# Performance work log

Hardware: AMD Instinct MI355X
Metric: run time of the kernel (lower is better)

Reference implementation:

```python
import jax, jax.numpy as jnp
import numpy as np

BN_EPS = 1e-5
NEG_SLOPE = 0.2


def _add_self_loops(edge_index, n):
    loops = jnp.arange(n, dtype=edge_index.dtype)
    src = jnp.concatenate([edge_index[0], loops])
    dst = jnp.concatenate([edge_index[1], loops])
    return src, dst


def _batchnorm(h, g, b):
    mean = h.mean(axis=0)
    var = h.var(axis=0)  # biased, as in BN forward
    return (h - mean) * jax.lax.rsqrt(var + BN_EPS) * g + b


def _gat_conv(x, edge_index, W, att_src, att_dst, bias):
    # heads=2, concat=False (mean over heads), add_self_loops=True
    n = x.shape[0]
    H, F = att_src.shape
    xp = (x @ W).reshape(n, H, F)                      # [N,H,F]
    a_src = jnp.einsum('nhf,hf->nh', xp, att_src)      # [N,H]
    a_dst = jnp.einsum('nhf,hf->nh', xp, att_dst)
    src, dst = _add_self_loops(edge_index, n)
    e = jax.nn.leaky_relu(a_src[src] + a_dst[dst], NEG_SLOPE)  # [Et,H]
    emax = jax.ops.segment_max(e, dst, num_segments=n)[dst]
    ex = jnp.exp(e - emax)
    denom = jax.ops.segment_sum(ex, dst, num_segments=n)[dst]
    alpha = ex / denom                                 # softmax per dst node
    msg = xp[src] * alpha[..., None]                   # [Et,H,F]
    out = jax.ops.segment_sum(msg, dst, num_segments=n)
    return out.mean(axis=1) + bias                     # [N,F]


def _gcn_conv(x, edge_index, W, bias):
    n = x.shape[0]
    xp = x @ W
    src, dst = _add_self_loops(edge_index, n)
    deg = jax.ops.segment_sum(jnp.ones_like(src, dtype=xp.dtype), dst, num_segments=n)
    dinv = jnp.where(deg > 0, jax.lax.rsqrt(jnp.maximum(deg, 1.0)), 0.0)
    norm = dinv[src] * dinv[dst]                       # [Et]
    out = jax.ops.segment_sum(xp[src] * norm[:, None], dst, num_segments=n)
    return out + bias


def setup_inputs() -> dict:
    key = jax.random.key(0)
    ks = jax.random.split(key, 16)
    N, E, D_IN, HID, LAT, DEC = 50000, 800000, 256, 128, 64, 256
    s = lambda fan: 1.0 / np.sqrt(fan)
    inp = {
        'x': jax.random.normal(ks[0], (N, D_IN), jnp.float32),
        'edge_index': jax.random.randint(ks[1], (2, E), 0, N, dtype=jnp.int32),
        'gat_W': jax.random.normal(ks[2], (D_IN, 2 * HID), jnp.float32) * s(D_IN),
        'gat_att_src': jax.random.normal(ks[3], (2, HID), jnp.float32) * s(HID),
        'gat_att_dst': jax.random.normal(ks[4], (2, HID), jnp.float32) * s(HID),
        'gat_bias': jnp.zeros((HID,), jnp.float32),
        'bn1_g': jnp.ones((HID,), jnp.float32),
        'bn1_b': jnp.zeros((HID,), jnp.float32),
        'gcn_W': jax.random.normal(ks[5], (HID, LAT), jnp.float32) * s(HID),
        'gcn_bias': jnp.zeros((LAT,), jnp.float32),
        'bn2_g': jnp.ones((LAT,), jnp.float32),
        'bn2_b': jnp.zeros((LAT,), jnp.float32),
        'mu_W': jax.random.normal(ks[6], (LAT, LAT), jnp.float32) * s(LAT),
        'mu_b': jnp.zeros((LAT,), jnp.float32),
        'lv_W': jax.random.normal(ks[7], (LAT, LAT), jnp.float32) * s(LAT),
        'lv_b': jnp.zeros((LAT,), jnp.float32),
        'res_W': jax.random.normal(ks[8], (LAT, LAT), jnp.float32) * s(LAT),
        'res_b': jnp.zeros((LAT,), jnp.float32),
        'dec_W1': jax.random.normal(ks[9], (2 * LAT, DEC), jnp.float32) * s(2 * LAT),
        'dec_b1': jnp.zeros((DEC,), jnp.float32),
        'dec_W2': jax.random.normal(ks[10], (DEC, 1), jnp.float32) * s(DEC),
        'dec_b2': jnp.zeros((1,), jnp.float32),
        'eps': jax.random.normal(ks[11], (N, LAT), jnp.float32),
    }
    return inp


def reference(x, edge_index, gat_W, gat_att_src, gat_att_dst, gat_bias,
              bn1_g, bn1_b, gcn_W, gcn_bias, bn2_g, bn2_b,
              mu_W, mu_b, lv_W, lv_b, res_W, res_b,
              dec_W1, dec_b1, dec_W2, dec_b2, eps):
    # encode (dropout omitted: eval mode; BN uses batch statistics)
    h = jax.nn.relu(_gat_conv(x, edge_index, gat_W, gat_att_src, gat_att_dst, gat_bias))
    h = _batchnorm(h, bn1_g, bn1_b)
    h = jax.nn.relu(_gcn_conv(h, edge_index, gcn_W, gcn_bias))
    h = _batchnorm(h, bn2_g, bn2_b)
    mu = h @ mu_W + mu_b
    logvar = h @ lv_W + lv_b
    # reparameterize
    z = mu + eps * jnp.exp(0.5 * logvar)
    # decode: edge-gather -> residual linear -> concat -> MLP
    res_z = z @ res_W + res_b
    row, col = edge_index[0], edge_index[1]
    e_emb = jnp.concatenate([res_z[row], res_z[col]], axis=1)  # [E, 2*LAT]
    hdec = jax.nn.relu(e_emb @ dec_W1 + dec_b1)
    recon = (hdec @ dec_W2 + dec_b2)[:, 0]
    return recon, mu, logvar
```

## Files before the change

kernel.cpp:

```cpp
#include <hip/hip_runtime.h>
#include <math.h>

constexpr int DIN = 256;
constexpr int HID = 128;
constexpr int LAT = 64;

typedef short bfrag __attribute__((ext_vector_type(8)));
typedef float f32x4 __attribute__((ext_vector_type(4)));

__device__ __forceinline__ float4 ld4(const float* p) { return *reinterpret_cast<const float4*>(p); }
__device__ __forceinline__ void st4(float* p, float4 v) { *reinterpret_cast<float4*>(p) = v; }

__device__ __forceinline__ unsigned short f2bf(float f) {
  unsigned int u = __float_as_uint(f);
  unsigned int r = (u + 0x7FFFu + ((u >> 16) & 1u)) >> 16;
  return (unsigned short)r;
}

__device__ __forceinline__ float bf2f(unsigned short u) {
  return __uint_as_float(((unsigned int)u) << 16);
}

__global__ __launch_bounds__(256) void gemm64(const float* __restrict__ A, const float* __restrict__ B,
                                              const float* __restrict__ crow, float* __restrict__ C,
                                              int M, int N, int K) {
  __shared__ float As[32][68];
  __shared__ float Bs[32][68];
  int t = threadIdx.x;
  int m0 = blockIdx.x * 64, n0 = blockIdx.y * 64;
  int tm = t & 15, tn = t >> 4;
  float acc[4][4];
#pragma unroll
  for (int i = 0; i < 4; i++)
#pragma unroll
    for (int j = 0; j < 4; j++) acc[i][j] = 0.f;

  for (int kt = 0; kt < K; kt += 32) {
#pragma unroll
    for (int i = 0; i < 2; ++i) {
      int f4 = t + i * 256;
      int m = f4 >> 3;
      int k4 = (f4 & 7) << 2;
      int gm = m0 + m;
      float4 v = make_float4(0.f, 0.f, 0.f, 0.f);
      if (gm < M) v = ld4(A + (size_t)gm * K + kt + k4);
      As[k4 + 0][m] = v.x; As[k4 + 1][m] = v.y; As[k4 + 2][m] = v.z; As[k4 + 3][m] = v.w;
    }
#pragma unroll
    for (int i = 0; i < 2; ++i) {
      int f4 = t + i * 256;
      int k = f4 >> 4;
      int n4 = (f4 & 15) << 2;
      float4 v = ld4(B + (size_t)(kt + k) * N + n0 + n4);
      st4(&Bs[k][n4], v);
    }
    __syncthreads();
#pragma unroll
    for (int k = 0; k < 32; ++k) {
      float4 a = ld4(&As[k][tm << 2]);
      float4 b = ld4(&Bs[k][tn << 2]);
      float av[4] = {a.x, a.y, a.z, a.w};
      float bv[4] = {b.x, b.y, b.z, b.w};
#pragma unroll
      for (int i = 0; i < 4; i++)
#pragma unroll
        for (int j = 0; j < 4; j++) acc[i][j] = fmaf(av[i], bv[j], acc[i][j]);
    }
    __syncthreads();
  }
#pragma unroll
  for (int i = 0; i < 4; ++i) {
    int gm = m0 + (tm << 2) + i;
    if (gm < M) {
      int nb = n0 + (tn << 2);
      float4 v = make_float4(acc[i][0], acc[i][1], acc[i][2], acc[i][3]);
      if (crow) { v.x += crow[nb]; v.y += crow[nb + 1]; v.z += crow[nb + 2]; v.w += crow[nb + 3]; }
      st4(C + (size_t)gm * N + nb, v);
    }
  }
}

__global__ __launch_bounds__(256) void gemm64b(const float* __restrict__ A, const float* __restrict__ B,
                                               const float* __restrict__ crow, unsigned short* __restrict__ Cb,
                                               int M, int N, int K) {
  __shared__ float As[32][68];
  __shared__ float Bs[32][68];
  int t = threadIdx.x;
  int m0 = blockIdx.x * 64, n0 = blockIdx.y * 64;
  int tm = t & 15, tn = t >> 4;
  float acc[4][4];
#pragma unroll
  for (int i = 0; i < 4; i++)
#pragma unroll
    for (int j = 0; j < 4; j++) acc[i][j] = 0.f;

  for (int kt = 0; kt < K; kt += 32) {
#pragma unroll
    for (int i = 0; i < 2; ++i) {
      int f4 = t + i * 256;
      int m = f4 >> 3;
      int k4 = (f4 & 7) << 2;
      int gm = m0 + m;
      float4 v = make_float4(0.f, 0.f, 0.f, 0.f);
      if (gm < M) v = ld4(A + (size_t)gm * K + kt + k4);
      As[k4 + 0][m] = v.x; As[k4 + 1][m] = v.y; As[k4 + 2][m] = v.z; As[k4 + 3][m] = v.w;
    }
#pragma unroll
    for (int i = 0; i < 2; ++i) {
      int f4 = t + i * 256;
      int k = f4 >> 4;
      int n4 = (f4 & 15) << 2;
      float4 v = ld4(B + (size_t)(kt + k) * N + n0 + n4);
      st4(&Bs[k][n4], v);
    }
    __syncthreads();
#pragma unroll
    for (int k = 0; k < 32; ++k) {
      float4 a = ld4(&As[k][tm << 2]);
      float4 b = ld4(&Bs[k][tn << 2]);
      float av[4] = {a.x, a.y, a.z, a.w};
      float bv[4] = {b.x, b.y, b.z, b.w};
#pragma unroll
      for (int i = 0; i < 4; i++)
#pragma unroll
        for (int j = 0; j < 4; j++) acc[i][j] = fmaf(av[i], bv[j], acc[i][j]);
    }
    __syncthreads();
  }
#pragma unroll
  for (int i = 0; i < 4; ++i) {
    int gm = m0 + (tm << 2) + i;
    if (gm < M) {
      int nb = n0 + (tn << 2);
      ushort4 o;
      o.x = f2bf(acc[i][0] + crow[nb]);
      o.y = f2bf(acc[i][1] + crow[nb + 1]);
      o.z = f2bf(acc[i][2] + crow[nb + 2]);
      o.w = f2bf(acc[i][3] + crow[nb + 3]);
      *(ushort4*)(Cb + (size_t)gm * N + nb) = o;
    }
  }
}

__global__ __launch_bounds__(256) void gemm_xp_mfma(const float* __restrict__ xf,
                                                    const unsigned short* __restrict__ Wtb,
                                                    unsigned short* __restrict__ xpb, int M) {
  __shared__ unsigned short Als[64 * 256];
  __shared__ unsigned short Bls[64 * 256];
  int t = threadIdx.x;
  int wv = t >> 6, l = t & 63, lg = l >> 4, ll = l & 15;
  int cg = blockIdx.x;
  int rt = blockIdx.y;

  {
    int row = t >> 2, seg = t & 3;
    int gr = min(rt * 64 + row, M - 1);
    const float4* src = (const float4*)(xf + (size_t)gr * 256 + seg * 64);
    int swz = (row & 7) << 4;
#pragma unroll
    for (int c = 0; c < 8; ++c) {
      float4 a = src[2 * c], b = src[2 * c + 1];
      uint4 v;
      v.x = (unsigned)f2bf(a.x) | ((unsigned)f2bf(a.y) << 16);
      v.y = (unsigned)f2bf(a.z) | ((unsigned)f2bf(a.w) << 16);
      v.z = (unsigned)f2bf(b.x) | ((unsigned)f2bf(b.y) << 16);
      v.w = (unsigned)f2bf(b.z) | ((unsigned)f2bf(b.w) << 16);
      int bo = seg * 128 + c * 16;
      *(uint4*)((char*)Als + row * 512 + (bo ^ swz)) = v;
    }
  }
  {
    int col = t >> 2, seg = t & 3;
    const uint4* src = (const uint4*)(Wtb + (size_t)(cg * 64 + col) * 256 + seg * 64);
    int swz = (col & 7) << 4;
#pragma unroll
    for (int c = 0; c < 8; ++c) {
      int bo = seg * 128 + c * 16;
      *(uint4*)((char*)Bls + col * 512 + (bo ^ swz)) = src[c];
    }
  }
  __syncthreads();

  f32x4 acc[4];
#pragma unroll
  for (int i = 0; i < 4; ++i) acc[i] = (f32x4){0.f, 0.f, 0.f, 0.f};

#pragma unroll
  for (int kt = 0; kt < 8; ++kt) {
    int ar = wv * 16 + ll;
    bfrag af = *(const bfrag*)((char*)Als + ar * 512 + ((kt * 64 + lg * 16) ^ ((ar & 7) << 4)));
#pragma unroll
    for (int fn = 0; fn < 4; ++fn) {
      int bc = fn * 16 + ll;
      bfrag bf = *(const bfrag*)((char*)Bls + bc * 512 + ((kt * 64 + lg * 16) ^ ((bc & 7) << 4)));
      acc[fn] = __builtin_amdgcn_mfma_f32_16x16x32_bf16(af, bf, acc[fn], 0, 0, 0);
    }
  }

#pragma unroll
  for (int fn = 0; fn < 4; ++fn) {
#pragma unroll
    for (int r = 0; r < 4; ++r) {
      int row = rt * 64 + wv * 16 + lg * 4 + r;
      if (row < M) xpb[(size_t)row * 512 + cg * 64 + fn * 16 + ll] = f2bf(acc[fn][r]);
    }
  }
}

__global__ __launch_bounds__(256) void attn_scores_bf(const unsigned short* __restrict__ xpb,
                                                      const float* __restrict__ att_src,
                                                      const float* __restrict__ att_dst,
                                                      float* __restrict__ a_src, float* __restrict__ a_dst, int N) {
  int wid = threadIdx.x >> 6, lane = threadIdx.x & 63;
  int n = blockIdx.x * 4 + wid;
  if (n >= N) return;
  int h = lane >> 5;
  int f4 = (lane & 31) << 2;
  ushort4 u = *(const ushort4*)(xpb + (size_t)n * 512 + lane * 4);
  float4 as = ld4(att_src + h * 128 + f4);
  float4 ad = ld4(att_dst + h * 128 + f4);
  float vx = bf2f(u.x), vy = bf2f(u.y), vz = bf2f(u.z), vw = bf2f(u.w);
  float ps = vx * as.x + vy * as.y + vz * as.z + vw * as.w;
  float pd = vx * ad.x + vy * ad.y + vz * ad.z + vw * ad.w;
#pragma unroll
  for (int m = 16; m >= 1; m >>= 1) { ps += __shfl_xor(ps, m); pd += __shfl_xor(pd, m); }
  if ((lane & 31) == 0) { a_src[n * 2 + h] = ps; a_dst[n * 2 + h] = pd; }
}

__global__ void deg_count(const int* __restrict__ ei, int E, int Et, int* __restrict__ deg) {
  int i = blockIdx.x * blockDim.x + threadIdx.x;
  if (i >= Et) return;
  int d = (i < E) ? ei[E + i] : (i - E);
  atomicAdd(&deg[d], 1);
}

__global__ __launch_bounds__(256) void bsum_kernel(const int* __restrict__ deg, int N, int* __restrict__ bsum) {
  int t = threadIdx.x;
  int i = blockIdx.x * 256 + t;
  int v = (i < N) ? deg[i] : 0;
#pragma unroll
  for (int m = 32; m >= 1; m >>= 1) v += __shfl_xor(v, m);
  __shared__ int sh[4];
  if ((t & 63) == 0) sh[t >> 6] = v;
  __syncthreads();
  if (t == 0) bsum[blockIdx.x] = sh[0] + sh[1] + sh[2] + sh[3];
}

__global__ __launch_bounds__(256) void bscan_kernel(int* __restrict__ bsum, int B) {
  __shared__ int sh[256];
  int t = threadIdx.x;
  int v = (t < B) ? bsum[t] : 0;
  sh[t] = v;
  __syncthreads();
  for (int d = 1; d < 256; d <<= 1) {
    int x = (t >= d) ? sh[t - d] : 0;
    __syncthreads();
    sh[t] += x;
    __syncthreads();
  }
  if (t < B) bsum[t] = sh[t] - v;
}

__global__ __launch_bounds__(256) void scan_apply(const int* __restrict__ deg, const int* __restrict__ bsum, int N,
                                                  int* __restrict__ offs, int* __restrict__ cursor,
                                                  float* __restrict__ dinv) {
  int t = threadIdx.x;
  int i = blockIdx.x * 256 + t;
  int v = (i < N) ? deg[i] : 0;
  __shared__ int sh[256];
  sh[t] = v;
  __syncthreads();
  for (int d = 1; d < 256; d <<= 1) {
    int x = (t >= d) ? sh[t - d] : 0;
    __syncthreads();
    sh[t] += x;
    __syncthreads();
  }
  if (i < N) {
    int off = bsum[blockIdx.x] + sh[t] - v;
    offs[i] = off;
    cursor[i] = off;
    dinv[i] = rsqrtf((float)v);
  }
}

__global__ void csr_fill(const int* __restrict__ ei, int E, int Et, int* __restrict__ cursor, int* __restrict__ csr) {
  int i = blockIdx.x * blockDim.x + threadIdx.x;
  if (i >= Et) return;
  int s, d;
  if (i < E) { s = ei[i]; d = ei[E + i]; } else { s = i - E; d = i - E; }
  int pos = atomicAdd(&cursor[d], 1);
  csr[pos] = s;
}

__global__ __launch_bounds__(256) void gat_fused(const int* __restrict__ offs, const int* __restrict__ deg,
                                                 const int* __restrict__ csr, const float* __restrict__ a_src,
                                                 const float* __restrict__ a_dst,
                                                 const unsigned short* __restrict__ xpb,
                                                 const float* __restrict__ bias,
                                                 float* __restrict__ h1, int N) {
  int wid = threadIdx.x >> 6, lane = threadIdx.x & 63;
  int n = blockIdx.x * 4 + wid;
  if (n >= N) return;
  int off = offs[n], dg = deg[n];
  float ad0 = a_dst[n * 2], ad1 = a_dst[n * 2 + 1];
  const float2* as2 = (const float2*)a_src;

  float4 acc = make_float4(0.f, 0.f, 0.f, 0.f);
  float s0 = 0.f, s1 = 0.f;
  bool h0 = lane < 32;

#define GAT_STEP(aa, uu)                                         \
  {                                                              \
    float e0 = (aa).x + ad0; e0 = e0 >= 0.f ? e0 : 0.2f * e0;    \
    float e1 = (aa).y + ad1; e1 = e1 >= 0.f ? e1 : 0.2f * e1;    \
    float x0 = __expf(e0), x1 = __expf(e1);                      \
    s0 += x0; s1 += x1;                                          \
    float xa = h0 ? x0 : x1;                                     \
    acc.x = fmaf(bf2f((uu).x), xa, acc.x);                       \
    acc.y = fmaf(bf2f((uu).y), xa, acc.y);                       \
    acc.z = fmaf(bf2f((uu).z), xa, acc.z);                       \
    acc.w = fmaf(bf2f((uu).w), xa, acc.w);                       \
  }

  int k = 0;
  for (; k + 4 <= dg; k += 4) {
    int sa = csr[off + k], sb = csr[off + k + 1], sc = csr[off + k + 2], sd = csr[off + k + 3];
    float2 aa = as2[sa], ab = as2[sb], ac = as2[sc], ad = as2[sd];
    ushort4 ua = ((const ushort4*)(xpb + (size_t)sa * 512))[lane];
    ushort4 ub = ((const ushort4*)(xpb + (size_t)sb * 512))[lane];
    ushort4 uc = ((const ushort4*)(xpb + (size_t)sc * 512))[lane];
    ushort4 ud = ((const ushort4*)(xpb + (size_t)sd * 512))[lane];
    GAT_STEP(aa, ua); GAT_STEP(ab, ub); GAT_STEP(ac, uc); GAT_STEP(ad, ud);
  }
  for (; k < dg; ++k) {
    int s = csr[off + k];
    float2 a = as2[s];
    ushort4 u = ((const ushort4*)(xpb + (size_t)s * 512))[lane];
    GAT_STEP(a, u);
  }
#undef GAT_STEP

  float r = h0 ? (1.f / s0) : (1.f / s1);
  acc.x *= r; acc.y *= r; acc.z *= r; acc.w *= r;

  float ox = __shfl_down(acc.x, 32);
  float oy = __shfl_down(acc.y, 32);
  float oz = __shfl_down(acc.z, 32);
  float ow = __shfl_down(acc.w, 32);
  if (h0) {
    int f4 = lane << 2;
    float4 b = ld4(bias + f4);
    float4 o;
    o.x = fmaxf(0.f, (acc.x + ox) * 0.5f + b.x);
    o.y = fmaxf(0.f, (acc.y + oy) * 0.5f + b.y);
    o.z = fmaxf(0.f, (acc.z + oz) * 0.5f + b.z);
    o.w = fmaxf(0.f, (acc.w + ow) * 0.5f + b.w);
    st4(h1 + (size_t)n * 128 + f4, o);
  }
}

template <int C>
__global__ __launch_bounds__(256) void bn_stats(const float* __restrict__ h, int N, float* __restrict__ P,
                                                float* __restrict__ PS) {
  constexpr int R = 256 / C;
  __shared__ float sh[256], sh2[256];
  int t = threadIdx.x;
  int c = t % C, r = t / C;
  float s = 0.f, ss = 0.f;
  for (int n = blockIdx.x * R + r; n < N; n += gridDim.x * R) {
    float v = h[(size_t)n * C + c];
    s += v; ss += v * v;
  }
  sh[t] = s; sh2[t] = ss;
  __syncthreads();
  if (r == 0) {
#pragma unroll
    for (int i = 1; i < R; ++i) { s += sh[i * C + c]; ss += sh2[i * C + c]; }
    P[blockIdx.x * C + c] = s;
    PS[blockIdx.x * C + c] = ss;
  }
}

__global__ __launch_bounds__(256) void bn_fold_gcn(const float* __restrict__ P, const float* __restrict__ PS,
                                                   int G, int N, const float* __restrict__ g,
                                                   const float* __restrict__ b, const float* __restrict__ W,
                                                   float* __restrict__ Wf, float* __restrict__ cvec) {
  __shared__ float ssv[128], stv[128];
  int t = threadIdx.x;
  if (t < 128) {
    float s = 0.f, ss = 0.f;
    for (int i = 0; i < G; ++i) { s += P[i * 128 + t]; ss += PS[i * 128 + t]; }
    float mean = s / N;
    float var = ss / N - mean * mean;
    float sc = g[t] * rsqrtf(var + 1e-5f);
    ssv[t] = sc;
    stv[t] = b[t] - mean * sc;
  }
  __syncthreads();
  for (int i = t; i < 128 * 64; i += 256) {
    int k = i >> 6;
    Wf[i] = ssv[k] * W[i];
  }
  if (t < 64) {
    float c = 0.f;
    for (int k = 0; k < 128; ++k) c += stv[k] * W[k * 64 + t];
    cvec[t] = c;
  }
}

__global__ __launch_bounds__(256) void bn_fold_mulv(const float* __restrict__ P, const float* __restrict__ PS,
                                                    int G, int N, const float* __restrict__ g,
                                                    const float* __restrict__ b,
                                                    const float* __restrict__ Wmu, const float* __restrict__ mub,
                                                    const float* __restrict__ Wlv, const float* __restrict__ lvb,
                                                    float* __restrict__ Wmuf, float* __restrict__ cmu,
                                                    float* __restrict__ Wlvf, float* __restrict__ clv) {
  __shared__ float ssv[64], stv[64];
  int t = threadIdx.x;
  if (t < 64) {
    float s = 0.f, ss = 0.f;
    for (int i = 0; i < G; ++i) { s += P[i * 64 + t]; ss += PS[i * 64 + t]; }
    float mean = s / N;
    float var = ss / N - mean * mean;
    float sc = g[t] * rsqrtf(var + 1e-5f);
    ssv[t] = sc;
    stv[t] = b[t] - mean * sc;
  }
  __syncthreads();
  for (int i = t; i < 4096; i += 256) {
    int k = i >> 6;
    Wmuf[i] = ssv[k] * Wmu[i];
    Wlvf[i] = ssv[k] * Wlv[i];
  }
  if (t < 64) {
    float cm = mub[t], cl = lvb[t];
    for (int k = 0; k < 64; ++k) { cm += stv[k] * Wmu[k * 64 + t]; cl += stv[k] * Wlv[k * 64 + t]; }
    cmu[t] = cm; clv[t] = cl;
  }
}

__global__ __launch_bounds__(256) void gcn_aggregate_bf(const int* __restrict__ offs, const int* __restrict__ deg,
                                                        const int* __restrict__ csr,
                                                        const unsigned short* __restrict__ xpb2,
                                                        const float* __restrict__ dinv, const float* __restrict__ bias,
                                                        float* __restrict__ g2, int N) {
  int wid = threadIdx.x >> 6, lane = threadIdx.x & 63;
  int n = blockIdx.x * 4 + wid;
  if (n >= N) return;
  int off = offs[n], dg = deg[n];
  float acc = 0.f;
  int k = 0;
  for (; k + 4 <= dg; k += 4) {
    int sa = csr[off + k], sb = csr[off + k + 1], sc = csr[off + k + 2], sd = csr[off + k + 3];
    float da = dinv[sa], db = dinv[sb], dc = dinv[sc], dd = dinv[sd];
    unsigned short ua = xpb2[(size_t)sa * 64 + lane];
    unsigned short ub = xpb2[(size_t)sb * 64 + lane];
    unsigned short uc = xpb2[(size_t)sc * 64 + lane];
    unsigned short ud = xpb2[(size_t)sd * 64 + lane];
    acc = fmaf(bf2f(ua), da, acc);
    acc = fmaf(bf2f(ub), db, acc);
    acc = fmaf(bf2f(uc), dc, acc);
    acc = fmaf(bf2f(ud), dd, acc);
  }
  for (; k < dg; ++k) {
    int s = csr[off + k];
    acc = fmaf(bf2f(xpb2[(size_t)s * 64 + lane]), dinv[s], acc);
  }
  float v = acc * dinv[n] + bias[lane];
  g2[(size_t)n * 64 + lane] = fmaxf(v, 0.f);
}

__global__ void reparam(const float* __restrict__ mu, const float* __restrict__ lv,
                        const float* __restrict__ eps, float* __restrict__ z, int total) {
  int i = blockIdx.x * blockDim.x + threadIdx.x;
  if (i >= total) return;
  z[i] = fmaf(eps[i], __expf(0.5f * lv[i]), mu[i]);
}

__global__ void prep_gatW(const float* __restrict__ W, unsigned short* __restrict__ Wtb) {
  int i = blockIdx.x * blockDim.x + threadIdx.x;
  if (i >= 256 * 256) return;
  int col = i >> 8, k = i & 255;
  Wtb[i] = f2bf(W[k * 256 + col]);
}

__global__ void prep_W1(const float* __restrict__ W1, unsigned short* __restrict__ W1t) {
  int i = blockIdx.x * blockDim.x + threadIdx.x;
  if (i >= 4 * 256 * 40) return;
  int kt = i / 10240;
  int rem = i - kt * 10240;
  int j = rem / 40;
  int kp = rem - j * 40;
  float v = (kp < 32) ? W1[(size_t)(kt * 32 + kp) * 256 + j] : 0.f;
  W1t[i] = f2bf(v);
}

__global__ __launch_bounds__(256) void decoder_mfma(const int* __restrict__ ei, int E,
                                                    const unsigned short* __restrict__ rzb,
                                                    const unsigned short* __restrict__ W1t,
                                                    const float* __restrict__ b1, const float* __restrict__ W2,
                                                    const float* __restrict__ b2, float* __restrict__ recon) {
  __shared__ unsigned short Als[64 * 128];
  __shared__ unsigned short Bls[256 * 40];
  __shared__ float red[4][64];
  int t = threadIdx.x;
  int wv = t >> 6, l = t & 63;
  int lg = l >> 4, ll = l & 15;
  int e0 = blockIdx.x * 64;

  {
    int e = t >> 2;
    int part = (t >> 1) & 1;
    int half = t & 1;
    int eg = e0 + e;
    if (eg >= E) eg = E - 1;
    int r = (part == 0) ? ei[eg] : ei[E + eg];
    const uint4* gsrc = (const uint4*)(rzb + (size_t)r * 64 + half * 32);
    int bo0 = part * 128 + half * 64;
    int swz = (e & 7) << 4;
#pragma unroll
    for (int c = 0; c < 4; ++c) {
      uint4 v = gsrc[c];
      int bo = bo0 + c * 16;
      *(uint4*)&Als[e * 128 + ((bo ^ swz) >> 1)] = v;
    }
  }

  f32x4 acc[4][4];
#pragma unroll
  for (int a = 0; a < 4; ++a)
#pragma unroll
    for (int b = 0; b < 4; ++b) acc[a][b] = (f32x4){0.f, 0.f, 0.f, 0.f};

  for (int kt = 0; kt < 4; ++kt) {
    __syncthreads();
    {
      const uint4* gsrc = (const uint4*)(W1t + kt * 10240);
      uint4* ldst = (uint4*)Bls;
#pragma unroll
      for (int i = 0; i < 5; ++i) ldst[t + i * 256] = gsrc[t + i * 256];
    }
    __syncthreads();

    bfrag af[4];
#pragma unroll
    for (int fm = 0; fm < 4; ++fm) {
      int e = fm * 16 + ll;
      int bo = kt * 64 + lg * 16;
      af[fm] = *(const bfrag*)&Als[e * 128 + ((bo ^ ((e & 7) << 4)) >> 1)];
    }
#pragma unroll
    for (int fn = 0; fn < 4; ++fn) {
      int j = wv * 64 + fn * 16 + ll;
      bfrag bf = *(const bfrag*)&Bls[j * 40 + lg * 8];
#pragma unroll
      for (int fm = 0; fm < 4; ++fm)
        acc[fm][fn] = __builtin_amdgcn_mfma_f32_16x16x32_bf16(af[fm], bf, acc[fm][fn], 0, 0, 0);
    }
  }

  float bj[4], wj[4];
#pragma unroll
  for (int fn = 0; fn < 4; ++fn) {
    int j = wv * 64 + fn * 16 + ll;
    bj[fn] = b1[j];
    wj[fn] = W2[j];
  }
#pragma unroll
  for (int fm = 0; fm < 4; ++fm) {
    float pr[4] = {0.f, 0.f, 0.f, 0.f};
#pragma unroll
    for (int fn = 0; fn < 4; ++fn) {
#pragma unroll
      for (int r = 0; r < 4; ++r)
        pr[r] = fmaf(fmaxf(acc[fm][fn][r] + bj[fn], 0.f), wj[fn], pr[r]);
    }
#pragma unroll
    for (int m = 8; m >= 1; m >>= 1) {
#pragma unroll
      for (int r = 0; r < 4; ++r) pr[r] += __shfl_xor(pr[r], m);
    }
    if (ll == 0) {
#pragma unroll
      for (int r = 0; r < 4; ++r) red[wv][fm * 16 + lg * 4 + r] = pr[r];
    }
  }
  __syncthreads();
  if (t < 64) {
    int eg = e0 + t;
    if (eg < E) recon[eg] = red[0][t] + red[1][t] + red[2][t] + red[3][t] + b2[0];
  }
}

extern "C" void kernel_launch(void* const* d_in, const int* in_sizes, int n_in,
                              void* d_out, int out_size, void* d_ws, size_t ws_size,
                              hipStream_t stream) {
  const float* x = (const float*)d_in[0];
  const int* ei = (const int*)d_in[1];
  const float* gat_W = (const float*)d_in[2];
  const float* att_src = (const float*)d_in[3];
  const float* att_dst = (const float*)d_in[4];
  const float* gat_bias = (const float*)d_in[5];
  const float* bn1_g = (const float*)d_in[6];
  const float* bn1_b = (const float*)d_in[7];
  const float* gcn_W = (const float*)d_in[8];
  const float* gcn_bias = (const float*)d_in[9];
  const float* bn2_g = (const float*)d_in[10];
  const float* bn2_b = (const float*)d_in[11];
  const float* mu_W = (const float*)d_in[12];
  const float* mu_b = (const float*)d_in[13];
  const float* lv_W = (const float*)d_in[14];
  const float* lv_b = (const float*)d_in[15];
  const float* res_W = (const float*)d_in[16];
  const float* res_b = (const float*)d_in[17];
  const float* dec_W1 = (const float*)d_in[18];
  const float* dec_b1 = (const float*)d_in[19];
  const float* dec_W2 = (const float*)d_in[20];
  const float* dec_b2 = (const float*)d_in[21];
  const float* eps = (const float*)d_in[22];

  int N = in_sizes[0] / DIN;
  int E = in_sizes[1] / 2;
  int Et = E + N;
  int NB = (N + 255) / 256;

  float* ws = (float*)d_ws;
  size_t off = 0;
  float* xp = ws; off += (size_t)N * 256;
  unsigned short* xpb = (unsigned short*)xp;
  unsigned short* xpb2 = (unsigned short*)xp;
  float* g2 = xp + (size_t)N * 64;
  float* zb = xp + (size_t)N * 128;
  float* rz = xp + (size_t)N * 192;
  unsigned short* rzb = (unsigned short*)rz;
  float* h1 = ws + off; off += (size_t)N * 128;
  float* a_src = ws + off; off += (size_t)2 * N;
  float* a_dst = ws + off; off += (size_t)2 * N;
  float* dinv = ws + off; off += N;
  float* P = ws + off; off += 128 * 128;
  float* PS = ws + off; off += 128 * 128;
  float* W2f = ws + off; off += 128 * 64;
  float* c2 = ws + off; off += 64;
  float* Wmuf = ws + off; off += 64 * 64;
  float* cmu = ws + off; off += 64;
  float* Wlvf = ws + off; off += 64 * 64;
  float* clv = ws + off; off += 64;
  unsigned short* W1t = (unsigned short*)(ws + off); off += 20480;
  unsigned short* Wtb = (unsigned short*)(ws + off); off += 32768;
  int* deg = (int*)(ws + off); off += N;
  int* offs = (int*)(ws + off); off += N;
  int* cursor = (int*)(ws + off); off += N;
  int* bsum = (int*)(ws + off); off += 256;
  int* csr = (int*)(ws + off); off += Et;

  float* recon = (float*)d_out;
  float* mu = recon + E;
  float* lv = mu + (size_t)N * LAT;

  prep_W1<<<(4 * 256 * 40 + 255) / 256, 256, 0, stream>>>(dec_W1, W1t);
  prep_gatW<<<(256 * 256 + 255) / 256, 256, 0, stream>>>(gat_W, Wtb);

  dim3 gX(4, (N + 63) / 64);
  gemm_xp_mfma<<<gX, 256, 0, stream>>>(x, Wtb, xpb, N);

  attn_scores_bf<<<(N + 3) / 4, 256, 0, stream>>>(xpb, att_src, att_dst, a_src, a_dst, N);

  hipMemsetAsync(deg, 0, (size_t)N * sizeof(int), stream);
  deg_count<<<(Et + 255) / 256, 256, 0, stream>>>(ei, E, Et, deg);
  bsum_kernel<<<NB, 256, 0, stream>>>(deg, N, bsum);
  bscan_kernel<<<1, 256, 0, stream>>>(bsum, NB);
  scan_apply<<<NB, 256, 0, stream>>>(deg, bsum, N, offs, cursor, dinv);
  csr_fill<<<(Et + 255) / 256, 256, 0, stream>>>(ei, E, Et, cursor, csr);

  gat_fused<<<(N + 3) / 4, 256, 0, stream>>>(offs, deg, csr, a_src, a_dst, xpb, gat_bias, h1, N);

  bn_stats<128><<<128, 256, 0, stream>>>(h1, N, P, PS);
  bn_fold_gcn<<<1, 256, 0, stream>>>(P, PS, 128, N, bn1_g, bn1_b, gcn_W, W2f, c2);
  dim3 gB((N + 63) / 64, 1);
  gemm64b<<<gB, 256, 0, stream>>>(h1, W2f, c2, xpb2, N, 64, 128);

  gcn_aggregate_bf<<<(N + 3) / 4, 256, 0, stream>>>(offs, deg, csr, xpb2, dinv, gcn_bias, g2, N);

  bn_stats<64><<<128, 256, 0, stream>>>(g2, N, P, PS);
  bn_fold_mulv<<<1, 256, 0, stream>>>(P, PS, 128, N, bn2_g, bn2_b, mu_W, mu_b, lv_W, lv_b,
                                      Wmuf, cmu, Wlvf, clv);
  gemm64<<<gB, 256, 0, stream>>>(g2, Wmuf, cmu, mu, N, 64, 64);
  gemm64<<<gB, 256, 0, stream>>>(g2, Wlvf, clv, lv, N, 64, 64);

  reparam<<<(N * 64 + 255) / 256, 256, 0, stream>>>(mu, lv, eps, zb, N * 64);
  gemm64b<<<gB, 256, 0, stream>>>(zb, res_W, res_b, rzb, N, 64, 64);

  decoder_mfma<<<(E + 63) / 64, 256, 0, stream>>>(ei, E, rzb, W1t, dec_b1, dec_W2, dec_b2, recon);
}
```

Measured before the change: 574.5 us.

## Fuse attention scores into GAT GEMM, fuse mu/logvar/reparam/residual tail, unroll gathers

Computes the GAT attention source and destination scores in the GEMM epilogue from fp32 accumulators. Partial sums across column tiles are combined with atomicAdd into zero-initialised buffers, so the separate score kernel and its re-read of xp go away. Replaces the two mu/logvar GEMMs, the reparam kernel and the residual GEMM with one tail kernel that keeps z in shared memory. It also adds 8-way unrolled gather loops in the GAT and GCN aggregation kernels for more memory-level parallelism, at the cost of extra launch memset, atomics and register pressure.

```diff
diff --git a/kernel.cpp b/kernel.cpp
--- a/kernel.cpp
+++ b/kernel.cpp
@@ -19,65 +19,6 @@
 
 __device__ __forceinline__ float bf2f(unsigned short u) {
   return __uint_as_float(((unsigned int)u) << 16);
-}
-
-__global__ __launch_bounds__(256) void gemm64(const float* __restrict__ A, const float* __restrict__ B,
-                                              const float* __restrict__ crow, float* __restrict__ C,
-                                              int M, int N, int K) {
-  __shared__ float As[32][68];
-  __shared__ float Bs[32][68];
-  int t = threadIdx.x;
-  int m0 = blockIdx.x * 64, n0 = blockIdx.y * 64;
-  int tm = t & 15, tn = t >> 4;
-  float acc[4][4];
-#pragma unroll
-  for (int i = 0; i < 4; i++)
-#pragma unroll
-    for (int j = 0; j < 4; j++) acc[i][j] = 0.f;
-
-  for (int kt = 0; kt < K; kt += 32) {
-#pragma unroll
-    for (int i = 0; i < 2; ++i) {
-      int f4 = t + i * 256;
-      int m = f4 >> 3;
-      int k4 = (f4 & 7) << 2;
-      int gm = m0 + m;
-      float4 v = make_float4(0.f, 0.f, 0.f, 0.f);
-      if (gm < M) v = ld4(A + (size_t)gm * K + kt + k4);
-      As[k4 + 0][m] = v.x; As[k4 + 1][m] = v.y; As[k4 + 2][m] = v.z; As[k4 + 3][m] = v.w;
-    }
-#pragma unroll
-    for (int i = 0; i < 2; ++i) {
-      int f4 = t + i * 256;
-      int k = f4 >> 4;
-      int n4 = (f4 & 15) << 2;
-      float4 v = ld4(B + (size_t)(kt + k) * N + n0 + n4);
-      st4(&Bs[k][n4], v);
-    }
-    __syncthreads();
-#pragma unroll
-    for (int k = 0; k < 32; ++k) {
-      float4 a = ld4(&As[k][tm << 2]);
-      float4 b = ld4(&Bs[k][tn << 2]);
-      float av[4] = {a.x, a.y, a.z, a.w};
-      float bv[4] = {b.x, b.y, b.z, b.w};
-#pragma unroll
-      for (int i = 0; i < 4; i++)
-#pragma unroll
-        for (int j = 0; j < 4; j++) acc[i][j] = fmaf(av[i], bv[j], acc[i][j]);
-    }
-    __syncthreads();
-  }
-#pragma unroll
-  for (int i = 0; i < 4; ++i) {
-    int gm = m0 + (tm << 2) + i;
-    if (gm < M) {
-      int nb = n0 + (tn << 2);
-      float4 v = make_float4(acc[i][0], acc[i][1], acc[i][2], acc[i][3]);
-      if (crow) { v.x += crow[nb]; v.y += crow[nb + 1]; v.z += crow[nb + 2]; v.w += crow[nb + 3]; }
-      st4(C + (size_t)gm * N + nb, v);
-    }
-  }
 }
 
 __global__ __launch_bounds__(256) void gemm64b(const float* __restrict__ A, const float* __restrict__ B,
@@ -144,7 +85,10 @@
 
 __global__ __launch_bounds__(256) void gemm_xp_mfma(const float* __restrict__ xf,
                                                     const unsigned short* __restrict__ Wtb,
-                                                    unsigned short* __restrict__ xpb, int M) {
+                                                    const float* __restrict__ att_src,
+                                                    const float* __restrict__ att_dst,
+                                                    unsigned short* __restrict__ xpb,
+                                                    float* __restrict__ a_src, float* __restrict__ a_dst, int M) {
   __shared__ unsigned short Als[64 * 256];
   __shared__ unsigned short Bls[64 * 256];
   int t = threadIdx.x;
@@ -205,26 +149,38 @@
       if (row < M) xpb[(size_t)row * 512 + cg * 64 + fn * 16 + ll] = f2bf(acc[fn][r]);
     }
   }
-}
-
-__global__ __launch_bounds__(256) void attn_scores_bf(const unsigned short* __restrict__ xpb,
-                                                      const float* __restrict__ att_src,
-                                                      const float* __restrict__ att_dst,
-                                                      float* __restrict__ a_src, float* __restrict__ a_dst, int N) {
-  int wid = threadIdx.x >> 6, lane = threadIdx.x & 63;
-  int n = blockIdx.x * 4 + wid;
-  if (n >= N) return;
-  int h = lane >> 5;
-  int f4 = (lane & 31) << 2;
-  ushort4 u = *(const ushort4*)(xpb + (size_t)n * 512 + lane * 4);
-  float4 as = ld4(att_src + h * 128 + f4);
-  float4 ad = ld4(att_dst + h * 128 + f4);
-  float vx = bf2f(u.x), vy = bf2f(u.y), vz = bf2f(u.z), vw = bf2f(u.w);
-  float ps = vx * as.x + vy * as.y + vz * as.z + vw * as.w;
-  float pd = vx * ad.x + vy * ad.y + vz * ad.z + vw * ad.w;
-#pragma unroll
-  for (int m = 16; m >= 1; m >>= 1) { ps += __shfl_xor(ps, m); pd += __shfl_xor(pd, m); }
-  if ((lane & 31) == 0) { a_src[n * 2 + h] = ps; a_dst[n * 2 + h] = pd; }
+
+  int h = cg >> 1;
+  int c0 = (cg & 1) * 64;
+  float asv[4], adv[4];
+#pragma unroll
+  for (int fn = 0; fn < 4; ++fn) {
+    asv[fn] = att_src[h * 128 + c0 + fn * 16 + ll];
+    adv[fn] = att_dst[h * 128 + c0 + fn * 16 + ll];
+  }
+  float ps[4] = {0.f, 0.f, 0.f, 0.f}, pd[4] = {0.f, 0.f, 0.f, 0.f};
+#pragma unroll
+  for (int fn = 0; fn < 4; ++fn)
+#pragma unroll
+    for (int r = 0; r < 4; ++r) {
+      ps[r] = fmaf(acc[fn][r], asv[fn], ps[r]);
+      pd[r] = fmaf(acc[fn][r], adv[fn], pd[r]);
+    }
+#pragma unroll
+  for (int m = 8; m >= 1; m >>= 1) {
+#pragma unroll
+    for (int r = 0; r < 4; ++r) { ps[r] += __shfl_xor(ps[r], m); pd[r] += __shfl_xor(pd[r], m); }
+  }
+  if (ll == 0) {
+#pragma unroll
+    for (int r = 0; r < 4; ++r) {
+      int row = rt * 64 + wv * 16 + lg * 4 + r;
+      if (row < M) {
+        atomicAdd(&a_src[row * 2 + h], ps[r]);
+        atomicAdd(&a_dst[row * 2 + h], pd[r]);
+      }
+    }
+  }
 }
 
 __global__ void deg_count(const int* __restrict__ ei, int E, int Et, int* __restrict__ deg) {
@@ -324,6 +280,19 @@
   }
 
   int k = 0;
+  for (; k + 8 <= dg; k += 8) {
+    int s_[8];
+#pragma unroll
+    for (int q = 0; q < 8; ++q) s_[q] = csr[off + k + q];
+    float2 a_[8];
+    ushort4 u_[8];
+#pragma unroll
+    for (int q = 0; q < 8; ++q) a_[q] = as2[s_[q]];
+#pragma unroll
+    for (int q = 0; q < 8; ++q) u_[q] = ((const ushort4*)(xpb + (size_t)s_[q] * 512))[lane];
+#pragma unroll
+    for (int q = 0; q < 8; ++q) GAT_STEP(a_[q], u_[q]);
+  }
   for (; k + 4 <= dg; k += 4) {
     int sa = csr[off + k], sb = csr[off + k + 1], sc = csr[off + k + 2], sd = csr[off + k + 3];
     float2 aa = as2[sa], ab = as2[sb], ac = as2[sc], ad = as2[sd];
@@ -451,6 +420,19 @@
   int off = offs[n], dg = deg[n];
   float acc = 0.f;
   int k = 0;
+  for (; k + 8 <= dg; k += 8) {
+    int s_[8];
+#pragma unroll
+    for (int q = 0; q < 8; ++q) s_[q] = csr[off + k + q];
+    float d_[8];
+    unsigned short u_[8];
+#pragma unroll
+    for (int q = 0; q < 8; ++q) d_[q] = dinv[s_[q]];
+#pragma unroll
+    for (int q = 0; q < 8; ++q) u_[q] = xpb2[(size_t)s_[q] * 64 + lane];
+#pragma unroll
+    for (int q = 0; q < 8; ++q) acc = fmaf(bf2f(u_[q]), d_[q], acc);
+  }
   for (; k + 4 <= dg; k += 4) {
     int sa = csr[off + k], sb = csr[off + k + 1], sc = csr[off + k + 2], sd = csr[off + k + 3];
     float da = dinv[sa], db = dinv[sb], dc = dinv[sc], dd = dinv[sd];
@@ -471,11 +453,120 @@
   g2[(size_t)n * 64 + lane] = fmaxf(v, 0.f);
 }
 
-__global__ void reparam(const float* __restrict__ mu, const float* __restrict__ lv,
-                        const float* __restrict__ eps, float* __restrict__ z, int total) {
-  int i = blockIdx.x * blockDim.x + threadIdx.x;
-  if (i >= total) return;
-  z[i] = fmaf(eps[i], __expf(0.5f * lv[i]), mu[i]);
+__global__ __launch_bounds__(256) void tail_fused(const float* __restrict__ g2,
+                                                  const float* __restrict__ Wmuf, const float* __restrict__ cmu,
+                                                  const float* __restrict__ Wlvf, const float* __restrict__ clv,
+                                                  const float* __restrict__ resW, const float* __restrict__ resb,
+                                                  const float* __restrict__ eps,
+                                                  float* __restrict__ mu, float* __restrict__ lv,
+                                                  unsigned short* __restrict__ rzb, int N) {
+  __shared__ float Gs[64][68];
+  __shared__ float Wm[64][64];
+  __shared__ float Wl[64][64];
+  __shared__ float Rw[64][64];
+  int t = threadIdx.x;
+  int m0 = blockIdx.x * 64;
+  int tm = t & 15, tn = t >> 4;
+
+#pragma unroll
+  for (int i = 0; i < 4; ++i) {
+    int f4 = t + i * 256;
+    int row = f4 >> 4;
+    int k4 = (f4 & 15) << 2;
+    int gr = m0 + row;
+    float4 v = make_float4(0.f, 0.f, 0.f, 0.f);
+    if (gr < N) v = ld4(g2 + (size_t)gr * 64 + k4);
+    Gs[k4 + 0][row] = v.x; Gs[k4 + 1][row] = v.y; Gs[k4 + 2][row] = v.z; Gs[k4 + 3][row] = v.w;
+    st4(&Wm[f4 >> 4][k4], ld4(Wmuf + f4 * 4));
+    st4(&Wl[f4 >> 4][k4], ld4(Wlvf + f4 * 4));
+    st4(&Rw[f4 >> 4][k4], ld4(resW + f4 * 4));
+  }
+  __syncthreads();
+
+  float am[4][4], al[4][4];
+#pragma unroll
+  for (int i = 0; i < 4; ++i)
+#pragma unroll
+    for (int j = 0; j < 4; ++j) { am[i][j] = 0.f; al[i][j] = 0.f; }
+
+#pragma unroll 8
+  for (int k = 0; k < 64; ++k) {
+    float4 a = ld4(&Gs[k][tm << 2]);
+    float4 bm = ld4(&Wm[k][tn << 2]);
+    float4 bl = ld4(&Wl[k][tn << 2]);
+    float av[4] = {a.x, a.y, a.z, a.w};
+    float bmv[4] = {bm.x, bm.y, bm.z, bm.w};
+    float blv[4] = {bl.x, bl.y, bl.z, bl.w};
+#pragma unroll
+    for (int i = 0; i < 4; ++i)
+#pragma unroll
+      for (int j = 0; j < 4; ++j) {
+        am[i][j] = fmaf(av[i], bmv[j], am[i][j]);
+        al[i][j] = fmaf(av[i], blv[j], al[i][j]);
+      }
+  }
+
+  int nb = tn << 2;
+  float cm4[4] = {cmu[nb], cmu[nb + 1], cmu[nb + 2], cmu[nb + 3]};
+  float cl4[4] = {clv[nb], clv[nb + 1], clv[nb + 2], clv[nb + 3]};
+  float zreg[4][4];
+#pragma unroll
+  for (int i = 0; i < 4; ++i) {
+    int gr = m0 + (tm << 2) + i;
+    if (gr < N) {
+      float4 ep = ld4(eps + (size_t)gr * 64 + nb);
+      float epv[4] = {ep.x, ep.y, ep.z, ep.w};
+      float muv[4], lvv[4];
+#pragma unroll
+      for (int j = 0; j < 4; ++j) {
+        muv[j] = am[i][j] + cm4[j];
+        lvv[j] = al[i][j] + cl4[j];
+        zreg[i][j] = fmaf(epv[j], __expf(0.5f * lvv[j]), muv[j]);
+      }
+      st4(mu + (size_t)gr * 64 + nb, make_float4(muv[0], muv[1], muv[2], muv[3]));
+      st4(lv + (size_t)gr * 64 + nb, make_float4(lvv[0], lvv[1], lvv[2], lvv[3]));
+    } else {
+#pragma unroll
+      for (int j = 0; j < 4; ++j) zreg[i][j] = 0.f;
+    }
+  }
+
+  __syncthreads();
+#pragma unroll
+  for (int i = 0; i < 4; ++i)
+#pragma unroll
+    for (int j = 0; j < 4; ++j) Gs[(tn << 2) + j][(tm << 2) + i] = zreg[i][j];
+  __syncthreads();
+
+  float ar[4][4];
+#pragma unroll
+  for (int i = 0; i < 4; ++i)
+#pragma unroll
+    for (int j = 0; j < 4; ++j) ar[i][j] = 0.f;
+#pragma unroll 8
+  for (int k = 0; k < 64; ++k) {
+    float4 a = ld4(&Gs[k][tm << 2]);
+    float4 b = ld4(&Rw[k][tn << 2]);
+    float av[4] = {a.x, a.y, a.z, a.w};
+    float bv[4] = {b.x, b.y, b.z, b.w};
+#pragma unroll
+    for (int i = 0; i < 4; ++i)
+#pragma unroll
+      for (int j = 0; j < 4; ++j) ar[i][j] = fmaf(av[i], bv[j], ar[i][j]);
+  }
+  float rb4[4] = {resb[nb], resb[nb + 1], resb[nb + 2], resb[nb + 3]};
+#pragma unroll
+  for (int i = 0; i < 4; ++i) {
+    int gr = m0 + (tm << 2) + i;
+    if (gr < N) {
+      ushort4 o;
+      o.x = f2bf(ar[i][0] + rb4[0]);
+      o.y = f2bf(ar[i][1] + rb4[1]);
+      o.z = f2bf(ar[i][2] + rb4[2]);
+      o.w = f2bf(ar[i][3] + rb4[3]);
+      *(ushort4*)(rzb + (size_t)gr * 64 + nb) = o;
+    }
+  }
 }
 
 __global__ void prep_gatW(const float* __restrict__ W, unsigned short* __restrict__ Wtb) {
@@ -631,7 +722,6 @@
   unsigned short* xpb = (unsigned short*)xp;
   unsigned short* xpb2 = (unsigned short*)xp;
   float* g2 = xp + (size_t)N * 64;
-  float* zb = xp + (size_t)N * 128;
   float* rz = xp + (size_t)N * 192;
   unsigned short* rzb = (unsigned short*)rz;
   float* h1 = ws + off; off += (size_t)N * 128;
@@ -660,11 +750,10 @@
 
   prep_W1<<<(4 * 256 * 40 + 255) / 256, 256, 0, stream>>>(dec_W1, W1t);
   prep_gatW<<<(256 * 256 + 255) / 256, 256, 0, stream>>>(gat_W, Wtb);
+  hipMemsetAsync(a_src, 0, (size_t)4 * N * sizeof(float), stream);
 
   dim3 gX(4, (N + 63) / 64);
-  gemm_xp_mfma<<<gX, 256, 0, stream>>>(x, Wtb, xpb, N);
-
-  attn_scores_bf<<<(N + 3) / 4, 256, 0, stream>>>(xpb, att_src, att_dst, a_src, a_dst, N);
+  gemm_xp_mfma<<<gX, 256, 0, stream>>>(x, Wtb, att_src, att_dst, xpb, a_src, a_dst, N);
 
   hipMemsetAsync(deg, 0, (size_t)N * sizeof(int), stream);
   deg_count<<<(Et + 255) / 256, 256, 0, stream>>>(ei, E, Et, deg);
@@ -685,11 +774,8 @@
   bn_stats<64><<<128, 256, 0, stream>>>(g2, N, P, PS);
   bn_fold_mulv<<<1, 256, 0, stream>>>(P, PS, 128, N, bn2_g, bn2_b, mu_W, mu_b, lv_W, lv_b,
                                       Wmuf, cmu, Wlvf, clv);
-  gemm64<<<gB, 256, 0, stream>>>(g2, Wmuf, cmu, mu, N, 64, 64);
-  gemm64<<<gB, 256, 0, stream>>>(g2, Wlvf, clv, lv, N, 64, 64);
-
-  reparam<<<(N * 64 + 255) / 256, 256, 0, stream>>>(mu, lv, eps, zb, N * 64);
-  gemm64b<<<gB, 256, 0, stream>>>(zb, res_W, res_b, rzb, N, 64, 64);
+  tail_fused<<<(N + 63) / 64, 256, 0, stream>>>(g2, Wmuf, cmu, Wlvf, clv, res_W, res_b, eps,
+                                                mu, lv, rzb, N);
 
   decoder_mfma<<<(E + 63) / 64, 256, 0, stream>>>(ei, E, rzb, W1t, dec_b1, dec_W2, dec_b2, recon);
 }
```

Measured after the change: 563.1 us, median of 2. -2.0%, faster.
